# Optimization experiments

Measured on AMD Instinct MI355X. Metric: run time of the kernel, lower is better.

Reference implementation:

```python
import jax, jax.numpy as jnp
import numpy as np

N, D = 16384, 32            # nodes, max neighbors (0-padded)
INP, U = 256, 128           # input_units, units
R, ENT = 8, 8               # relations, entity types (relation/entity id 0 = padding for relations)


def setup_inputs() -> dict:
    key = jax.random.key(0)
    ks = jax.random.split(key, 12)
    s = 0.05  # scale learned params for numerical sanity (torch init is raw randn)
    return {
        "node_state": jax.random.normal(ks[0], (N, INP), dtype=jnp.float32),
        "adjacency": jax.random.randint(ks[1], (N, D), 0, N + 1, dtype=jnp.int32),  # 0 = pad row
        "point_enc": jax.random.randint(ks[2], (N,), 0, ENT, dtype=jnp.int32),
        "relation_enc": jax.random.randint(ks[3], (N, D), 0, R, dtype=jnp.int32),   # 0 = pad edge
        "point_enc_w": jax.random.normal(ks[4], (ENT, INP, U), dtype=jnp.float32) * s,
        "relation_enc_w": jax.random.normal(ks[5], (R, U, U), dtype=jnp.float32) * s,
        "q_w": jax.random.normal(ks[6], (U, U), dtype=jnp.float32) * s,
        "k_w": jax.random.normal(ks[7], (U, U), dtype=jnp.float32) * s,
        "v_w": jax.random.normal(ks[8], (U, U), dtype=jnp.float32) * s,
        "fc_w": jax.random.normal(ks[9], (U, U), dtype=jnp.float32) * s,
        "fc_b": jax.random.normal(ks[10], (U,), dtype=jnp.float32) * s,
    }


def reference(node_state, adjacency, point_enc, relation_enc,
              point_enc_w, relation_enc_w, q_w, k_w, v_w, fc_w, fc_b):
    ent, inp, u = point_enc_w.shape
    r_cnt = relation_enc_w.shape[0]
    dt = node_state.dtype

    # center = node_state @ point_enc_w[point_enc]; loop over small fixed entity set
    # to avoid materializing an (N, INP, U) gathered weight tensor.
    center = jnp.zeros((node_state.shape[0], u), dtype=dt)
    for e in range(ent):
        center = center + jnp.where(point_enc[:, None] == e,
                                    node_state @ point_enc_w[e], 0.0)

    # prepend zero row: adjacency index 0 == padding neighbor
    padded = jnp.concatenate([jnp.zeros((1, u), dtype=dt), center], axis=0)  # (N+1, U)
    x = padded[adjacency]  # (N, D, U) gathered neighbor embeddings

    # neighbors = x @ relation_enc_w[relation_enc]; per-relation GEMM + mask
    # (same math as the per-edge gathered matmul, without the E*U*U blowup)
    neighbors = jnp.zeros_like(x)
    for r in range(r_cnt):
        neighbors = neighbors + jnp.where(relation_enc[..., None] == r,
                                          jnp.einsum('ndu,uv->ndv', x, relation_enc_w[r]), 0.0)

    scale = u ** 0.5
    q = (center @ q_w) / scale                               # (N, U)
    k = jnp.einsum('ndu,uv->ndv', neighbors, k_w) / scale    # (N, D, U)
    v = jnp.einsum('ndu,uv->ndv', neighbors, v_w)            # (N, D, U)

    scores = jnp.einsum('nu,ndu->nd', q, k)                  # (N, D)
    scores = jnp.where(relation_enc == 0, jnp.asarray(-1e9, dt), scores)
    attn = jax.nn.softmax(scores, axis=-1)                   # over neighbors
    agg = jnp.einsum('nd,ndu->nu', attn, v)                  # (N, U)

    return center + jax.nn.relu(agg @ fc_w + fc_b)           # (N, U)
```

## Files before the change

kernel.cpp:

```cpp
#include <hip/hip_runtime.h>

#define NNODE 16384
#define DD 32
#define INPC 256
#define UC 128
#define RC 8
#define EC 8

typedef __attribute__((ext_vector_type(8))) short short8;
typedef __attribute__((ext_vector_type(4))) float float4v;
typedef __attribute__((ext_vector_type(4))) unsigned uint4v;

__device__ __forceinline__ unsigned short f2bf(float f) {
    unsigned u = __builtin_bit_cast(unsigned, f);
    unsigned r = (u + 0x7FFFu + ((u >> 16) & 1u)) >> 16;
    return (unsigned short)r;
}
__device__ __forceinline__ float bf2f(unsigned short s) { return __builtin_bit_cast(float, (unsigned)s << 16); }

__device__ __forceinline__ short8 ld8bf(const float* p) {
    float4 v0 = *(const float4*)p;
    float4 v1 = *(const float4*)(p + 4);
    short8 a;
    a[0] = (short)f2bf(v0.x); a[1] = (short)f2bf(v0.y);
    a[2] = (short)f2bf(v0.z); a[3] = (short)f2bf(v0.w);
    a[4] = (short)f2bf(v1.x); a[5] = (short)f2bf(v1.y);
    a[6] = (short)f2bf(v1.z); a[7] = (short)f2bf(v1.w);
    return a;
}

__device__ __forceinline__ int bfrag_idx(int k, int col, int nct) {
    int ks = k >> 5, ct = col >> 4;
    int l = (((k >> 3) & 3) << 4) | (col & 15);
    return (((ks * nct + ct) << 6) + l) * 8 + (k & 7);
}

__global__ void k_setup(const float* __restrict__ pew, const float* __restrict__ qw,
                        const float* __restrict__ kw, const float* __restrict__ relw,
                        const float* __restrict__ vw, const float* __restrict__ fcw,
                        const int* __restrict__ pe,
                        unsigned short* __restrict__ pewfrag,
                        unsigned short* __restrict__ BallQfrag, unsigned short* __restrict__ RVFfrag,
                        int* __restrict__ blockhist) {
    __shared__ unsigned short stage_s[128 * 132];
    __shared__ unsigned short mat_s[16 * 136];
    __shared__ int hh[8];
    int b = blockIdx.x;
    if (b < 1024) {
        int id = b * 256 + threadIdx.x;
        int e = id >> 15, k = (id >> 7) & 255, col = id & 127;
        pewfrag[(e << 15) + bfrag_idx(k, col, 8)] = f2bf(pew[id]);
        return;
    }
    if (b < 1088) {
        int pb = b - 1024;
        int r = pb & 7, i0 = (pb >> 3) * 16;
        int w = threadIdx.x >> 6, l = threadIdx.x & 63;
        int mrow = l & 15, kgrp = (l >> 4) << 3;
        const float* R = relw + r * (UC * UC);

        float4v accP[2] = {};
        #pragma unroll
        for (int ks = 0; ks < 4; ++ks) {
            short8 a = ld8bf(&qw[(i0 + mrow) * UC + ks * 32 + kgrp]);
            #pragma unroll
            for (int ci = 0; ci < 2; ++ci) {
                int ct = w * 2 + ci;
                short8 bf = ld8bf(&kw[(ct * 16 + mrow) * UC + ks * 32 + kgrp]);
                accP[ci] = __builtin_amdgcn_mfma_f32_16x16x32_bf16(a, bf, accP[ci], 0, 0, 0);
            }
        }
        #pragma unroll
        for (int ci = 0; ci < 2; ++ci)
            #pragma unroll
            for (int reg = 0; reg < 4; ++reg) {
                int row = ((l >> 4) << 2) + reg;
                int col = (w * 2 + ci) * 16 + mrow;
                mat_s[row * 136 + col] = f2bf(accP[ci][reg] * (1.0f / 128.0f));
            }
        for (int it = 0; it < 16; ++it) {
            int idx = it * 256 + threadIdx.x;
            int row = idx >> 5, col = (idx & 31) * 4;
            float4 v = *(const float4*)&vw[row * UC + col];
            uint2 o;
            o.x = (unsigned)f2bf(v.x) | ((unsigned)f2bf(v.y) << 16);
            o.y = (unsigned)f2bf(v.z) | ((unsigned)f2bf(v.w) << 16);
            *(uint2*)&stage_s[row * 132 + col] = o;
        }
        __syncthreads();

        float4v accM[2] = {}, accV[2] = {};
        #pragma unroll
        for (int ks = 0; ks < 4; ++ks) {
            short8 aM = *(const short8*)&mat_s[mrow * 136 + ks * 32 + kgrp];
            short8 aV = ld8bf(&R[(i0 + mrow) * UC + ks * 32 + kgrp]);
            #pragma unroll
            for (int ci = 0; ci < 2; ++ci) {
                int ct = w * 2 + ci;
                short8 bM = ld8bf(&R[(ct * 16 + mrow) * UC + ks * 32 + kgrp]);
                accM[ci] = __builtin_amdgcn_mfma_f32_16x16x32_bf16(aM, bM, accM[ci], 0, 0, 0);
                uint4v pv;
                #pragma unroll
                for (int jp = 0; jp < 4; ++jp) {
                    unsigned e0 = stage_s[(ks * 32 + kgrp + jp * 2) * 132 + ct * 16 + mrow];
                    unsigned e1 = stage_s[(ks * 32 + kgrp + jp * 2 + 1) * 132 + ct * 16 + mrow];
                    pv[jp] = e0 | (e1 << 16);
                }
                accV[ci] = __builtin_amdgcn_mfma_f32_16x16x32_bf16(
                    aV, __builtin_bit_cast(short8, pv), accV[ci], 0, 0, 0);
            }
        }
        #pragma unroll
        for (int ci = 0; ci < 2; ++ci)
            #pragma unroll
            for (int reg = 0; reg < 4; ++reg) {
                int i = i0 + ((l >> 4) << 2) + reg;
                int col = r * 128 + (w * 2 + ci) * 16 + mrow;
                BallQfrag[bfrag_idx(i, col, 64)] = f2bf(accM[ci][reg]);
            }
        __syncthreads();
        #pragma unroll
        for (int ci = 0; ci < 2; ++ci)
            #pragma unroll
            for (int reg = 0; reg < 4; ++reg)
                mat_s[(((l >> 4) << 2) + reg) * 136 + (w * 2 + ci) * 16 + mrow] = f2bf(accV[ci][reg]);
        for (int it = 0; it < 16; ++it) {
            int idx = it * 256 + threadIdx.x;
            int row = idx >> 5, col = (idx & 31) * 4;
            float4 v = *(const float4*)&fcw[row * UC + col];
            uint2 o;
            o.x = (unsigned)f2bf(v.x) | ((unsigned)f2bf(v.y) << 16);
            o.y = (unsigned)f2bf(v.z) | ((unsigned)f2bf(v.w) << 16);
            *(uint2*)&stage_s[row * 132 + col] = o;
        }
        __syncthreads();

        float4v accF[2] = {};
        #pragma unroll
        for (int ks = 0; ks < 4; ++ks) {
            short8 aF = *(const short8*)&mat_s[mrow * 136 + ks * 32 + kgrp];
            #pragma unroll
            for (int ci = 0; ci < 2; ++ci) {
                int ct = w * 2 + ci;
                uint4v pv;
                #pragma unroll
                for (int jp = 0; jp < 4; ++jp) {
                    unsigned e0 = stage_s[(ks * 32 + kgrp + jp * 2) * 132 + ct * 16 + mrow];
                    unsigned e1 = stage_s[(ks * 32 + kgrp + jp * 2 + 1) * 132 + ct * 16 + mrow];
                    pv[jp] = e0 | (e1 << 16);
                }
                accF[ci] = __builtin_amdgcn_mfma_f32_16x16x32_bf16(
                    aF, __builtin_bit_cast(short8, pv), accF[ci], 0, 0, 0);
            }
        }
        #pragma unroll
        for (int ci = 0; ci < 2; ++ci)
            #pragma unroll
            for (int reg = 0; reg < 4; ++reg) {
                int i = i0 + ((l >> 4) << 2) + reg;
                int col = (w * 2 + ci) * 16 + mrow;
                RVFfrag[bfrag_idx(r * 128 + i, col, 8)] = f2bf(accF[ci][reg]);
            }
        return;
    }
    {
        int hb = b - 1088;
        if (threadIdx.x < 8) hh[threadIdx.x] = 0;
        __syncthreads();
        atomicAdd(&hh[pe[hb * 256 + threadIdx.x]], 1);
        __syncthreads();
        if (threadIdx.x < 8) blockhist[hb * 8 + threadIdx.x] = hh[threadIdx.x];
    }
}

__global__ void k_scatter(const int* __restrict__ pe, const int* __restrict__ blockhist,
                          int* __restrict__ list, int* __restrict__ cnt, int* __restrict__ basep) {
    __shared__ int boff[8];
    __shared__ int totS[8], exS[8];
    __shared__ int wavecnt[4 * 8];
    int t = threadIdx.x, w = t >> 6, l = t & 63;
    if (w == 0) {
        #pragma unroll
        for (int e = 0; e < 8; ++e) {
            int h = blockhist[l * 8 + e];
            int pref = h;
            #pragma unroll
            for (int off = 1; off < 64; off <<= 1) {
                int v = __shfl_up(pref, off, 64);
                pref += (l >= off) ? v : 0;
            }
            if (l == (int)blockIdx.x) exS[e] = pref - h;
            if (l == 63) totS[e] = pref;
        }
    }
    __syncthreads();
    if (t == 0) {
        int run = 0;
        #pragma unroll
        for (int e = 0; e < 8; ++e) {
            boff[e] = run + exS[e];
            if (blockIdx.x == 0) { basep[e] = run; cnt[e] = totS[e]; }
            run += totS[e];
        }
    }
    __syncthreads();
    int n = blockIdx.x * 256 + t;
    int e = pe[n];
    unsigned long long mymask = 0;
    #pragma unroll
    for (int r = 0; r < 8; ++r) {
        unsigned long long m = __ballot(e == r);
        if (e == r) mymask = m;
        if (l == r) wavecnt[w * 8 + r] = (int)__popcll(m);
    }
    __syncthreads();
    int off = 0;
    for (int w2 = 0; w2 < w; ++w2) off += wavecnt[w2 * 8 + e];
    unsigned long long ltmask = (1ull << l) - 1ull;
    int rank = (int)__popcll(mymask & ltmask);
    list[boff[e] + off + rank] = n;
}

__global__ __launch_bounds__(256, 4)
void k_center(const float* __restrict__ ns, const unsigned short* __restrict__ pewfrag,
              const int* __restrict__ list, const int* __restrict__ cnt,
              const int* __restrict__ base, unsigned short* __restrict__ center_bf) {
    int e = blockIdx.y;
    int c = cnt[e];
    int start = blockIdx.x * 16;
    if (start >= c) return;
    int w = threadIdx.x >> 6, l = threadIdx.x & 63;

    int rid = list[base[e] + min(start + (l & 15), c - 1)];

    float4v acc[2] = {};
    const unsigned short* pf = pewfrag + ((size_t)e << 15);
    #pragma unroll
    for (int ks = 0; ks < 8; ++ks) {
        short8 a = ld8bf(&ns[(size_t)rid * 256 + ks * 32 + ((l >> 4) << 3)]);
        #pragma unroll
        for (int ci = 0; ci < 2; ++ci) {
            int ct = w * 2 + ci;
            short8 b = *(const short8*)&pf[(((ks * 8 + ct) << 6) + l) * 8];
            acc[ci] = __builtin_amdgcn_mfma_f32_16x16x32_bf16(a, b, acc[ci], 0, 0, 0);
        }
    }
    #pragma unroll
    for (int reg = 0; reg < 4; ++reg) {
        int row16 = start + ((l >> 4) << 2) + reg;
        if (row16 < c) {
            int gid = list[base[e] + row16];
            #pragma unroll
            for (int ci = 0; ci < 2; ++ci)
                center_bf[(size_t)gid * 128 + (w * 2 + ci) * 16 + (l & 15)] = f2bf(acc[ci][reg]);
        }
    }
}

#define QSTRIDE 1096
__global__ __launch_bounds__(256, 4)
void k_final(const unsigned short* __restrict__ center_bf,
             const unsigned short* __restrict__ BallQfrag,
             const unsigned short* __restrict__ RVFfrag,
             const int* __restrict__ adj, const int* __restrict__ rel,
             const float* __restrict__ fcb, float* __restrict__ out) {
    __shared__ unsigned short qlds[16 * QSTRIDE];
    __shared__ uint2 edata[4][32];
    int w = threadIdx.x >> 6, l = threadIdx.x & 63;
    int n0 = blockIdx.x * 16;

    {
        short8 a[4];
        #pragma unroll
        for (int ks = 0; ks < 4; ++ks)
            a[ks] = *(const short8*)&center_bf[(size_t)(n0 + (l & 15)) * 128 + ks * 32 + ((l >> 4) << 3)];
        for (int ci = 0; ci < 16; ++ci) {
            int ct = w * 16 + ci;
            float4v acc = {};
            #pragma unroll
            for (int ks = 0; ks < 4; ++ks) {
                short8 b = *(const short8*)&BallQfrag[(((ks * 64 + ct) << 6) + l) * 8];
                acc = __builtin_amdgcn_mfma_f32_16x16x32_bf16(a[ks], b, acc, 0, 0, 0);
            }
            int r = ct >> 3;
            int ch = (ct & 7) * 16 + (l & 15);
            #pragma unroll
            for (int reg = 0; reg < 4; ++reg) {
                int rn = ((l >> 4) << 2) + reg;
                qlds[rn * QSTRIDE + r * 136 + ch] = f2bf(acc[reg]);
            }
        }
    }
    __syncthreads();

    for (int q = 0; q < 4; ++q) {
        int tn = w * 4 + q;
        int n = n0 + tn;
        int ai[2], rv[2], rowv[2];
        #pragma unroll
        for (int t = 0; t < 2; ++t) {
            ai[t] = adj[n * DD + t * 16 + (l & 15)];
            rv[t] = rel[n * DD + t * 16 + (l & 15)];
            rowv[t] = ai[t] > 0 ? ai[t] - 1 : 0;
        }
        float4v sc[2] = {};
        #pragma unroll
        for (int ks = 0; ks < 4; ++ks) {
            short8 qb = *(const short8*)&qlds[tn * QSTRIDE + (l & 7) * 136 + ks * 32 + ((l >> 4) << 3)];
            #pragma unroll
            for (int t = 0; t < 2; ++t) {
                short8 xa = *(const short8*)&center_bf[(size_t)rowv[t] * 128 + ks * 32 + ((l >> 4) << 3)];
                sc[t] = __builtin_amdgcn_mfma_f32_16x16x32_bf16(xa, qb, sc[t], 0, 0, 0);
            }
        }
        float sel[2][4];
        int ai2[2][4];
        #pragma unroll
        for (int t = 0; t < 2; ++t)
            #pragma unroll
            for (int reg = 0; reg < 4; ++reg) {
                int e2l = ((l >> 4) & 3) * 4 + reg;
                int rd2 = __shfl(rv[t], (l & 48) | e2l, 64);
                ai2[t][reg] = __shfl(ai[t], (l & 48) | e2l, 64);
                float s = __shfl(sc[t][reg], (l & 48) | rd2, 64);
                if (ai2[t][reg] == 0) s = 0.f;
                if (rd2 == 0) s = -1e9f;
                sel[t][reg] = s;
            }
        float mx = sel[0][0];
        #pragma unroll
        for (int t = 0; t < 2; ++t)
            #pragma unroll
            for (int reg = 0; reg < 4; ++reg) mx = fmaxf(mx, sel[t][reg]);
        mx = fmaxf(mx, __shfl_xor(mx, 16, 64));
        mx = fmaxf(mx, __shfl_xor(mx, 32, 64));
        float at[2][4];
        float sm = 0.f;
        #pragma unroll
        for (int t = 0; t < 2; ++t)
            #pragma unroll
            for (int reg = 0; reg < 4; ++reg) {
                at[t][reg] = __expf(sel[t][reg] - mx);
                sm += at[t][reg];
            }
        sm += __shfl_xor(sm, 16, 64);
        sm += __shfl_xor(sm, 32, 64);
        float inv = 1.0f / sm;
        #pragma unroll
        for (int t = 0; t < 2; ++t)
            #pragma unroll
            for (int reg = 0; reg < 4; ++reg) {
                at[t][reg] *= inv;
                if (ai2[t][reg] == 0) at[t][reg] = 0.f;
            }

        #pragma unroll
        for (int rg = 0; rg < 4; ++rg) {
            if (l == (l >> 4) * 20 + rg) {
                #pragma unroll
                for (int t = 0; t < 2; ++t) {
                    uint2 md;
                    md.x = (unsigned)rowv[t];
                    md.y = (unsigned)f2bf(at[t][rg]) | ((unsigned)rv[t] << 16);
                    edata[w][t * 16 + (l & 15)] = md;
                }
            }
        }

        unsigned aw[4];
        int rows[8];
        #pragma unroll
        for (int jp = 0; jp < 4; ++jp) {
            uint2 m0 = edata[w][((l >> 4) << 3) + jp * 2];
            uint2 m1 = edata[w][((l >> 4) << 3) + jp * 2 + 1];
            unsigned s0 = ((m0.y >> 16) == (unsigned)(l & 15)) ? (m0.y & 0xFFFFu) : 0u;
            unsigned s1 = ((m1.y >> 16) == (unsigned)(l & 15)) ? (m1.y & 0xFFFFu) : 0u;
            aw[jp] = s0 | (s1 << 16);
            rows[jp * 2] = (int)m0.x;
            rows[jp * 2 + 1] = (int)m1.x;
        }
        uint4v av = {aw[0], aw[1], aw[2], aw[3]};
        short8 afrag = __builtin_bit_cast(short8, av);
        const unsigned short* xb0 = center_bf + (size_t)rows[0] * 128 + (l & 15);
        const unsigned short* xb1 = center_bf + (size_t)rows[1] * 128 + (l & 15);
        const unsigned short* xb2 = center_bf + (size_t)rows[2] * 128 + (l & 15);
        const unsigned short* xb3 = center_bf + (size_t)rows[3] * 128 + (l & 15);
        const unsigned short* xb4 = center_bf + (size_t)rows[4] * 128 + (l & 15);
        const unsigned short* xb5 = center_bf + (size_t)rows[5] * 128 + (l & 15);
        const unsigned short* xb6 = center_bf + (size_t)rows[6] * 128 + (l & 15);
        const unsigned short* xb7 = center_bf + (size_t)rows[7] * 128 + (l & 15);
        #pragma unroll
        for (int ct = 0; ct < 8; ++ct) {
            unsigned p0 = xb0[ct * 16], p1 = xb1[ct * 16], p2 = xb2[ct * 16], p3 = xb3[ct * 16];
            unsigned p4 = xb4[ct * 16], p5 = xb5[ct * 16], p6 = xb6[ct * 16], p7 = xb7[ct * 16];
            uint4v bv = {p0 | (p1 << 16), p2 | (p3 << 16), p4 | (p5 << 16), p6 | (p7 << 16)};
            float4v zc = {};
            float4v acc = __builtin_amdgcn_mfma_f32_16x16x32_bf16(
                afrag, __builtin_bit_cast(short8, bv), zc, 0, 0, 0);
            if (l < 32) {
                int rbase = (l >> 4) << 2;
                #pragma unroll
                for (int reg = 0; reg < 4; ++reg)
                    qlds[tn * QSTRIDE + (rbase + reg) * 136 + ct * 16 + (l & 15)] = f2bf(acc[reg]);
            }
        }
    }
    __syncthreads();

    #pragma unroll
    for (int ci = 0; ci < 2; ++ci) {
        int ct = w * 2 + ci;
        float4v acc = {};
        #pragma unroll 4
        for (int ks = 0; ks < 32; ++ks) {
            short8 a = *(const short8*)&qlds[(l & 15) * QSTRIDE + (ks >> 2) * 136
                                             + (ks & 3) * 32 + ((l >> 4) << 3)];
            short8 b = *(const short8*)&RVFfrag[(((ks * 8 + ct) << 6) + l) * 8];
            acc = __builtin_amdgcn_mfma_f32_16x16x32_bf16(a, b, acc, 0, 0, 0);
        }
        int col = ct * 16 + (l & 15);
        float bb = fcb[col];
        #pragma unroll
        for (int reg = 0; reg < 4; ++reg) {
            int n = n0 + ((l >> 4) << 2) + reg;
            float v = acc[reg] + bb;
            v = v > 0.f ? v : 0.f;
            out[(size_t)n * 128 + col] = bf2f(center_bf[(size_t)n * 128 + col]) + v;
        }
    }
}

extern "C" void kernel_launch(void* const* d_in, const int* in_sizes, int n_in,
                              void* d_out, int out_size, void* d_ws, size_t ws_size,
                              hipStream_t stream) {
    const float* node_state = (const float*)d_in[0];
    const int*   adjacency  = (const int*)d_in[1];
    const int*   point_enc  = (const int*)d_in[2];
    const int*   relation   = (const int*)d_in[3];
    const float* pew        = (const float*)d_in[4];
    const float* relw       = (const float*)d_in[5];
    const float* qw         = (const float*)d_in[6];
    const float* kw         = (const float*)d_in[7];
    const float* vw         = (const float*)d_in[8];
    const float* fcw        = (const float*)d_in[9];
    const float* fcb        = (const float*)d_in[10];
    float* out = (float*)d_out;

    char* ws = (char*)d_ws;
    unsigned short* BallQfrag = (unsigned short*)ws;  ws += 128 * 1024 * 2;
    unsigned short* RVFfrag   = (unsigned short*)ws;  ws += 1024 * 128 * 2;
    unsigned short* center_bf = (unsigned short*)ws;  ws += (size_t)NNODE * 128 * 2;
    unsigned short* pewfrag   = (unsigned short*)ws;  ws += 8 * 32768 * 2;
    int* blockhist            = (int*)ws;             ws += 64 * 8 * 4;
    int* cnt                  = (int*)ws;             ws += 32;
    int* basep                = (int*)ws;             ws += 32;
    int* list                 = (int*)ws;             ws += NNODE * 4;

    k_setup<<<1152, 256, 0, stream>>>(pew, qw, kw, relw, vw, fcw, point_enc,
                                      pewfrag, BallQfrag, RVFfrag, blockhist);
    k_scatter<<<64, 256, 0, stream>>>(point_enc, blockhist, list, cnt, basep);
    k_center<<<dim3(192, 8), 256, 0, stream>>>(node_state, pewfrag, list, cnt, basep, center_bf);
    k_final<<<NNODE / 16, 256, 0, stream>>>(center_bf, BallQfrag, RVFfrag,
                                            adjacency, relation, fcb, out);
}
```

Baseline: 166.5 us.

## Stage gathered neighbor rows in swizzled LDS with register prefetch in k_final

Each node's 32 gathered neighbor rows are loaded once from global memory with coalesced 16-byte vector loads into a per-wave, XOR-swizzled LDS tile. The next node's rows are prefetched into registers while the current node is processed. Both the score MFMA and the aggregation MFMA now read their operands from LDS, where before each did its own scattered 2-byte global gathers. Adjacency and relation indices are also loaded up front. The extra LDS and registers lower the launch-bounds occupancy hint from 4 to 2 blocks per SM, which can reduce latency hiding.

```diff
diff --git a/kernel.cpp b/kernel.cpp
--- a/kernel.cpp
+++ b/kernel.cpp
@@ -258,16 +258,40 @@
 }
 
 #define QSTRIDE 1096
-__global__ __launch_bounds__(256, 4)
+__global__ __launch_bounds__(256, 2)
 void k_final(const unsigned short* __restrict__ center_bf,
              const unsigned short* __restrict__ BallQfrag,
              const unsigned short* __restrict__ RVFfrag,
              const int* __restrict__ adj, const int* __restrict__ rel,
              const float* __restrict__ fcb, float* __restrict__ out) {
     __shared__ unsigned short qlds[16 * QSTRIDE];
-    __shared__ uint2 edata[4][32];
+    __shared__ __align__(16) unsigned short xs[4][4096];
+    __shared__ unsigned edata[4][32];
     int w = threadIdx.x >> 6, l = threadIdx.x & 63;
     int n0 = blockIdx.x * 16;
+
+    int aiq[4][2], rvq[4][2], myrow[4];
+    #pragma unroll
+    for (int q = 0; q < 4; ++q) {
+        int n = n0 + w * 4 + q;
+        #pragma unroll
+        for (int t = 0; t < 2; ++t) {
+            aiq[q][t] = adj[n * DD + t * 16 + (l & 15)];
+            rvq[q][t] = rel[n * DD + t * 16 + (l & 15)];
+        }
+    }
+    #pragma unroll
+    for (int q = 0; q < 4; ++q) {
+        int r0 = aiq[q][0] > 0 ? aiq[q][0] - 1 : 0;
+        int r1 = aiq[q][1] > 0 ? aiq[q][1] - 1 : 0;
+        int s0 = __shfl(r0, (l >> 1) & 15, 64);
+        int s1 = __shfl(r1, (l >> 1) & 15, 64);
+        myrow[q] = (l >= 32) ? s1 : s0;
+    }
+    uint4v sb[8];
+    #pragma unroll
+    for (int i = 0; i < 8; ++i)
+        sb[i] = *(const uint4v*)&center_bf[(size_t)myrow[0] * 128 + ((l & 1) + 2 * i) * 8];
 
     {
         short8 a[4];
@@ -293,23 +317,31 @@
     }
     __syncthreads();
 
+    #pragma unroll
     for (int q = 0; q < 4; ++q) {
         int tn = w * 4 + q;
-        int n = n0 + tn;
-        int ai[2], rv[2], rowv[2];
-        #pragma unroll
-        for (int t = 0; t < 2; ++t) {
-            ai[t] = adj[n * DD + t * 16 + (l & 15)];
-            rv[t] = rel[n * DD + t * 16 + (l & 15)];
-            rowv[t] = ai[t] > 0 ? ai[t] - 1 : 0;
-        }
+        int ai[2] = {aiq[q][0], aiq[q][1]};
+        int rv[2] = {rvq[q][0], rvq[q][1]};
+
+        #pragma unroll
+        for (int i = 0; i < 8; ++i)
+            *(uint4v*)&xs[w][i * 512 + (l >> 3) * 64
+                             + ((((l >> 1) & 3) ^ ((l >> 3) & 3))) * 16 + (l & 1) * 8] = sb[i];
+        if (q < 3) {
+            #pragma unroll
+            for (int i = 0; i < 8; ++i)
+                sb[i] = *(const uint4v*)&center_bf[(size_t)myrow[q + 1] * 128 + ((l & 1) + 2 * i) * 8];
+        }
+
         float4v sc[2] = {};
         #pragma unroll
         for (int ks = 0; ks < 4; ++ks) {
             short8 qb = *(const short8*)&qlds[tn * QSTRIDE + (l & 7) * 136 + ks * 32 + ((l >> 4) << 3)];
             #pragma unroll
             for (int t = 0; t < 2; ++t) {
-                short8 xa = *(const short8*)&center_bf[(size_t)rowv[t] * 128 + ks * 32 + ((l >> 4) << 3)];
+                short8 xa = *(const short8*)&xs[w][(2 * ks + (l >> 5)) * 512
+                                  + (4 * t + ((l >> 2) & 3)) * 64
+                                  + (((l & 3) ^ ((l >> 2) & 3))) * 16 + ((l >> 4) & 1) * 8];
                 sc[t] = __builtin_amdgcn_mfma_f32_16x16x32_bf16(xa, qb, sc[t], 0, 0, 0);
             }
         }
@@ -358,42 +390,36 @@
         for (int rg = 0; rg < 4; ++rg) {
             if (l == (l >> 4) * 20 + rg) {
                 #pragma unroll
-                for (int t = 0; t < 2; ++t) {
-                    uint2 md;
-                    md.x = (unsigned)rowv[t];
-                    md.y = (unsigned)f2bf(at[t][rg]) | ((unsigned)rv[t] << 16);
-                    edata[w][t * 16 + (l & 15)] = md;
-                }
+                for (int t = 0; t < 2; ++t)
+                    edata[w][t * 16 + (l & 15)] = (unsigned)f2bf(at[t][rg]) | ((unsigned)rv[t] << 16);
             }
         }
 
         unsigned aw[4];
-        int rows[8];
         #pragma unroll
         for (int jp = 0; jp < 4; ++jp) {
-            uint2 m0 = edata[w][((l >> 4) << 3) + jp * 2];
-            uint2 m1 = edata[w][((l >> 4) << 3) + jp * 2 + 1];
-            unsigned s0 = ((m0.y >> 16) == (unsigned)(l & 15)) ? (m0.y & 0xFFFFu) : 0u;
-            unsigned s1 = ((m1.y >> 16) == (unsigned)(l & 15)) ? (m1.y & 0xFFFFu) : 0u;
+            unsigned m0 = edata[w][((l >> 4) << 3) + jp * 2];
+            unsigned m1 = edata[w][((l >> 4) << 3) + jp * 2 + 1];
+            unsigned s0 = ((m0 >> 16) == (unsigned)(l & 15)) ? (m0 & 0xFFFFu) : 0u;
+            unsigned s1 = ((m1 >> 16) == (unsigned)(l & 15)) ? (m1 & 0xFFFFu) : 0u;
             aw[jp] = s0 | (s1 << 16);
-            rows[jp * 2] = (int)m0.x;
-            rows[jp * 2 + 1] = (int)m1.x;
         }
         uint4v av = {aw[0], aw[1], aw[2], aw[3]};
         short8 afrag = __builtin_bit_cast(short8, av);
-        const unsigned short* xb0 = center_bf + (size_t)rows[0] * 128 + (l & 15);
-        const unsigned short* xb1 = center_bf + (size_t)rows[1] * 128 + (l & 15);
-        const unsigned short* xb2 = center_bf + (size_t)rows[2] * 128 + (l & 15);
-        const unsigned short* xb3 = center_bf + (size_t)rows[3] * 128 + (l & 15);
-        const unsigned short* xb4 = center_bf + (size_t)rows[4] * 128 + (l & 15);
-        const unsigned short* xb5 = center_bf + (size_t)rows[5] * 128 + (l & 15);
-        const unsigned short* xb6 = center_bf + (size_t)rows[6] * 128 + (l & 15);
-        const unsigned short* xb7 = center_bf + (size_t)rows[7] * 128 + (l & 15);
+
         #pragma unroll
         for (int ct = 0; ct < 8; ++ct) {
-            unsigned p0 = xb0[ct * 16], p1 = xb1[ct * 16], p2 = xb2[ct * 16], p3 = xb3[ct * 16];
-            unsigned p4 = xb4[ct * 16], p5 = xb5[ct * 16], p6 = xb6[ct * 16], p7 = xb7[ct * 16];
-            uint4v bv = {p0 | (p1 << 16), p2 | (p3 << 16), p4 | (p5 << 16), p6 | (p7 << 16)};
+            unsigned short p[8];
+            #pragma unroll
+            for (int jj = 0; jj < 8; ++jj) {
+                int st = (l >> 4) * 2 + (jj >> 2);
+                int slot = (jj & 3) ^ (st & 3);
+                p[jj] = xs[w][ct * 512 + st * 64 + slot * 16 + (l & 15)];
+            }
+            uint4v bv = {(unsigned)p[0] | ((unsigned)p[1] << 16),
+                         (unsigned)p[2] | ((unsigned)p[3] << 16),
+                         (unsigned)p[4] | ((unsigned)p[5] << 16),
+                         (unsigned)p[6] | ((unsigned)p[7] << 16)};
             float4v zc = {};
             float4v acc = __builtin_amdgcn_mfma_f32_16x16x32_bf16(
                 afrag, __builtin_bit_cast(short8, bv), zc, 0, 0, 0);
```

Result: faster. 160.2 us (-3.8%).
